# Kernel optimization log

Hardware: AMD Instinct MI355X
Metric: run time of the kernel (lower is better)

## Reference

```python
import jax, jax.numpy as jnp
import numpy as np

H = 2048       # hidden_size
I = 5504       # intermediate_size
E = 8          # num_experts
TOPK = 2       # num_experts_per_tok


def setup_inputs() -> dict:
    key = jax.random.key(0)
    ks = jax.random.split(key, 5)
    s = 0.02
    x = jax.random.normal(ks[0], (2, 2048, H), dtype=jnp.float32)
    router_w = jax.random.normal(ks[1], (E, H), dtype=jnp.float32) * s   # Linear weight [out,in]
    Wg = jax.random.normal(ks[2], (E, I, H), dtype=jnp.float32) * s      # gate_proj per expert
    Wu = jax.random.normal(ks[3], (E, I, H), dtype=jnp.float32) * s      # up_proj per expert
    Wd = jax.random.normal(ks[4], (E, H, I), dtype=jnp.float32) * s      # down_proj per expert
    return {"x": x, "router_w": router_w, "Wg": Wg, "Wu": Wu, "Wd": Wd}


def reference(x, router_w, Wg, Wu, Wd):
    B, S, Hh = x.shape
    xf = x.reshape(-1, Hh)                                  # [T, H]
    logits = xf @ router_w.T                                # [T, E]
    top_vals, top_idx = jax.lax.top_k(logits, TOPK)         # [T, K]
    top_w = jax.nn.softmax(top_vals, axis=-1)               # softmax over selected logits only
    # combine weight per (token, expert): zero if expert not selected
    combine = jnp.sum(jax.nn.one_hot(top_idx, E, dtype=xf.dtype) * top_w[..., None], axis=1)  # [T, E]

    out = jnp.zeros_like(xf)
    for e in range(E):  # fixed small expert loop (unrolled under jit)
        h = jax.nn.silu(xf @ Wg[e].T) * (xf @ Wu[e].T)      # [T, I]
        y = h @ Wd[e].T                                     # [T, H]
        out = out + combine[:, e:e + 1] * y
    return out.reshape(B, S, Hh)
```

## Files before the change

kernel.cpp:

```cpp
#include <hip/hip_runtime.h>
#include <cstdint>
#include <cstddef>

#define HDIM 2048
#define IDIM 5504
#define NEXP 8
#define NTOK 4096
#define NROWS (2 * NTOK)

#define NCT1 86
#define NRT1 10
#define NWG1 (NCT1 * NRT1 * NEXP)
#define NCT2 16
#define NRT2 10
#define NWG2 (NCT2 * NRT2 * NEXP)

typedef _Float16 half8 __attribute__((ext_vector_type(8)));
typedef _Float16 half4v __attribute__((ext_vector_type(4)));
typedef float floatx4 __attribute__((ext_vector_type(4)));

#define GLOAD16(g, l)                                                         \
  __builtin_amdgcn_global_load_lds(                                           \
      (const __attribute__((address_space(1))) void*)(g),                     \
      (__attribute__((address_space(3))) void*)(l), 16, 0, 0)

#define XH_OFF   0
#define HB_OFF   (XH_OFF + (size_t)NTOK * HDIM * 2)
#define BTOK_OFF (HB_OFF + (size_t)NROWS * IDIM * 2)
#define BW_OFF   (BTOK_OFF + 32768)
#define TOKP_OFF (BW_OFF + 32768)
#define TOKW_OFF (TOKP_OFF + 16384)
#define T2R_OFF  (TOKW_OFF + 32768)
#define META_OFF (T2R_OFF + 32768)
#define Y2_OFF   (META_OFF + 128)


__global__ void cvt_x_kernel(const float4* __restrict__ x, half4v* __restrict__ xh, int n4) {
  int i = blockIdx.x * blockDim.x + threadIdx.x;
  int st = gridDim.x * blockDim.x;
  for (; i < n4; i += st) {
    float4 v = x[i];
    half4v o = { (_Float16)v.x, (_Float16)v.y, (_Float16)v.z, (_Float16)v.w };
    xh[i] = o;
  }
}

__global__ void router_kernel(const float* __restrict__ x, const float* __restrict__ rw,
                              int* __restrict__ tokp, float2* __restrict__ tokw,
                              int* __restrict__ cnt) {
  int t = blockIdx.x * 4 + (threadIdx.x >> 6);
  int lane = threadIdx.x & 63;
  const float4* xr = (const float4*)(x + (size_t)t * HDIM);
  float acc[NEXP];
#pragma unroll
  for (int e = 0; e < NEXP; ++e) acc[e] = 0.f;
#pragma unroll
  for (int it = 0; it < HDIM / 256; ++it) {
    float4 xv = xr[lane + 64 * it];
#pragma unroll
    for (int e = 0; e < NEXP; ++e) {
      float4 wv = ((const float4*)(rw + (size_t)e * HDIM))[lane + 64 * it];
      acc[e] += xv.x * wv.x + xv.y * wv.y + xv.z * wv.z + xv.w * wv.w;
    }
  }
#pragma unroll
  for (int off = 32; off > 0; off >>= 1) {
#pragma unroll
    for (int e = 0; e < NEXP; ++e) acc[e] += __shfl_xor(acc[e], off);
  }
  if (lane == 0) {
    int e0 = 0; float v0 = acc[0];
#pragma unroll
    for (int e = 1; e < NEXP; ++e) {
      if (acc[e] > v0) { v0 = acc[e]; e0 = e; }
    }
    int e1 = -1; float v1 = -3.0e38f;
#pragma unroll
    for (int e = 0; e < NEXP; ++e) {
      if (e == e0) continue;
      if (acc[e] > v1) { v1 = acc[e]; e1 = e; }
    }
    float w0 = 1.f / (1.f + __expf(v1 - v0));
    tokp[t] = e0 | (e1 << 8);
    tokw[t] = make_float2(w0, 1.f - w0);
    atomicAdd(&cnt[e0], 1);
    atomicAdd(&cnt[e1], 1);
  }
}

__global__ void scan_kernel(const int* __restrict__ cnt, int* __restrict__ offp) {
  if (threadIdx.x == 0) {
    int s = 0;
    for (int e = 0; e < NEXP; ++e) { offp[e] = s; s += cnt[e]; }
    offp[NEXP] = s;
  }
}

__global__ void scatter_kernel(const int* __restrict__ tokp, const float2* __restrict__ tokw,
                               const int* __restrict__ offp, int* __restrict__ cursor,
                               int* __restrict__ btok, float* __restrict__ bw,
                               int* __restrict__ t2r) {
  int t = blockIdx.x * blockDim.x + threadIdx.x;
  if (t >= NTOK) return;
  int p = tokp[t];
  float2 w = tokw[t];
  int e0 = p & 0xff, e1 = (p >> 8) & 0xff;
  int r0 = offp[e0] + atomicAdd(&cursor[e0], 1);
  btok[r0] = t; bw[r0] = w.x; t2r[2 * t] = r0;
  int r1 = offp[e1] + atomicAdd(&cursor[e1], 1);
  btok[r1] = t; bw[r1] = w.y; t2r[2 * t + 1] = r1;
}

__global__ void combine_kernel(const _Float16* __restrict__ y2, const int* __restrict__ t2r,
                               const float2* __restrict__ tokw, float* __restrict__ out) {
  int idx = blockIdx.x * 256 + threadIdx.x;
  int t = idx >> 9, c = (idx & 511) * 4;
  int r0 = t2r[2 * t], r1 = t2r[2 * t + 1];
  float2 w = tokw[t];
  half4v v0 = *(const half4v*)(y2 + (size_t)r0 * HDIM + c);
  half4v v1 = *(const half4v*)(y2 + (size_t)r1 * HDIM + c);
  float4 o;
  o.x = w.x * (float)v0[0] + w.y * (float)v1[0];
  o.y = w.x * (float)v0[1] + w.y * (float)v1[1];
  o.z = w.x * (float)v0[2] + w.y * (float)v1[2];
  o.w = w.x * (float)v0[3] + w.y * (float)v1[3];
  *(float4*)(out + (size_t)t * HDIM + c) = o;
}

__global__ __launch_bounds__(256, 3) void stage1_kernel(
    const _Float16* __restrict__ xh, const float* __restrict__ Wg, const float* __restrict__ Wu,
    const int* __restrict__ offp, const int* __restrict__ btok, _Float16* __restrict__ hb) {
  int bid = blockIdx.x;
  int wg = (bid & 7) * (NWG1 / 8) + (bid >> 3);
  int rt = wg % NRT1;
  int ct = (wg / NRT1) % NCT1;
  int e  = wg / (NRT1 * NCT1);
  int base = offp[e];
  int ne = offp[e + 1] - base;
  if (rt * 128 >= ne) return;
  int valid = ne - rt * 128; if (valid > 128) valid = 128;
  int tid = threadIdx.x, lane = tid & 63, wave = tid >> 6;

  __shared__ __attribute__((aligned(16))) _Float16 As[2][128 * 32];
  __shared__ __attribute__((aligned(16))) _Float16 Bs[2][128 * 32];

  const char* abase = (const char*)xh;
  uint32_t aoffB[2];
  const float* bsrc[2];
  int bdstB[2];
  size_t eoff = (size_t)e * IDIM * HDIM;
#pragma unroll
  for (int i = 0; i < 2; ++i) {
    int L = wave * 128 + i * 64 + lane;
    int u = L >> 3, sc = (L & 7) ^ (u & 7);
    int r = 2 * u + (sc >> 2), q = sc & 3;
    int rr = (r < valid) ? r : (valid - 1);
    aoffB[i] = (uint32_t)(((uint32_t)btok[base + rt * 128 + rr] * HDIM + q * 8) * 2);
    const float* rp = (r < 64) ? (Wg + eoff + (size_t)(ct * 64 + r) * HDIM)
                               : (Wu + eoff + (size_t)(ct * 64 + (r - 64)) * HDIM);
    bsrc[i] = rp + q * 8;
    bdstB[i] = L * 16;
  }
  int adst0 = __builtin_amdgcn_readfirstlane(wave * 2048);

  int wm = wave >> 1, wn = wave & 1;
  int lrow = lane & 15, kg = lane >> 4;

  int aoff[4], boff[4];
#pragma unroll
  for (int mi = 0; mi < 4; ++mi) {
    int r = wm * 64 + mi * 16 + lrow;
    int u = r >> 1, cc = (r & 1) * 4 + kg;
    aoff[mi] = u * 64 + ((cc ^ (u & 7)) * 8);
  }
#pragma unroll
  for (int f = 0; f < 4; ++f) {
    int rb = (f < 2) ? (wn * 32 + f * 16 + lrow) : (64 + wn * 32 + (f - 2) * 16 + lrow);
    int u = rb >> 1, cc = (rb & 1) * 4 + kg;
    boff[f] = u * 64 + ((cc ^ (u & 7)) * 8);
  }

  floatx4 acc[4][4] = {};
  floatx4 bp[2][2];

  auto bload = [&](int t) {
#pragma unroll
    for (int i = 0; i < 2; ++i) {
      bp[i][0] = *(const floatx4*)(bsrc[i] + t * 32);
      bp[i][1] = *(const floatx4*)(bsrc[i] + t * 32 + 4);
    }
  };
  auto astage = [&](int t, int buf) {
    uint32_t kb = (uint32_t)t * 64u;
#pragma unroll
    for (int i = 0; i < 2; ++i)
      GLOAD16(abase + (aoffB[i] + kb), (char*)As[buf] + adst0 + i * 1024);
  };
  auto bwrite = [&](int buf) {
#pragma unroll
    for (int i = 0; i < 2; ++i) {
      half8 h = { (_Float16)bp[i][0].x, (_Float16)bp[i][0].y, (_Float16)bp[i][0].z, (_Float16)bp[i][0].w,
                  (_Float16)bp[i][1].x, (_Float16)bp[i][1].y, (_Float16)bp[i][1].z, (_Float16)bp[i][1].w };
      *(half8*)((char*)Bs[buf] + bdstB[i]) = h;
    }
  };
  auto compute = [&](int buf) {
    half8 af[4], bf[4];
#pragma unroll
    for (int mi = 0; mi < 4; ++mi) af[mi] = *(const half8*)&As[buf][aoff[mi]];
#pragma unroll
    for (int f = 0; f < 4; ++f) bf[f] = *(const half8*)&Bs[buf][boff[f]];
#pragma unroll
    for (int mi = 0; mi < 4; ++mi)
#pragma unroll
      for (int f = 0; f < 4; ++f)
        acc[mi][f] = __builtin_amdgcn_mfma_f32_16x16x32_f16(af[mi], bf[f], acc[mi][f], 0, 0, 0);
  };

  int cur = 0;
  bload(0);
  astage(0, 0);
  bwrite(0);
  __syncthreads();
#pragma unroll 2
  for (int t = 0; t < HDIM / 32 - 1; ++t) {
    bload(t + 1);
    astage(t + 1, cur ^ 1);
    compute(cur);
    bwrite(cur ^ 1);
    __syncthreads();
    cur ^= 1;
  }
  compute(cur);

  size_t hrow_base = (size_t)(base + rt * 128);
#pragma unroll
  for (int mi = 0; mi < 4; ++mi) {
#pragma unroll
    for (int j = 0; j < 4; ++j) {
      int r = wm * 64 + mi * 16 + kg * 4 + j;
      if (r < valid) {
#pragma unroll
        for (int f = 0; f < 2; ++f) {
          float g = acc[mi][f][j], u = acc[mi][f + 2][j];
          float hv = g / (1.f + __expf(-g)) * u;
          int c = ct * 64 + wn * 32 + f * 16 + lrow;
          hb[(hrow_base + r) * IDIM + c] = (_Float16)hv;
        }
      }
    }
  }
}

__global__ __launch_bounds__(256, 3) void stage2_kernel(
    const _Float16* __restrict__ hb, const float* __restrict__ Wd,
    const int* __restrict__ offp, _Float16* __restrict__ y2) {
  int bid = blockIdx.x;
  int wg = (bid & 7) * (NWG2 / 8) + (bid >> 3);
  int rt = wg % NRT2;
  int ct = (wg / NRT2) % NCT2;
  int e  = wg / (NRT2 * NCT2);
  int base = offp[e];
  int ne = offp[e + 1] - base;
  if (rt * 128 >= ne) return;
  int valid = ne - rt * 128; if (valid > 128) valid = 128;
  int tid = threadIdx.x, lane = tid & 63, wave = tid >> 6;

  __shared__ __attribute__((aligned(16))) _Float16 As[2][128 * 32];
  __shared__ __attribute__((aligned(16))) _Float16 Bs[2][128 * 32];

  const char* abase = (const char*)hb;
  uint32_t aoffB[2];
  const float* bsrc[2];
  int bdstB[2];
  const float* wdE = Wd + (size_t)e * HDIM * IDIM;
#pragma unroll
  for (int i = 0; i < 2; ++i) {
    int L = wave * 128 + i * 64 + lane;
    int u = L >> 3, sc = (L & 7) ^ (u & 7);
    int r = 2 * u + (sc >> 2), q = sc & 3;
    int rr = (r < valid) ? r : (valid - 1);
    aoffB[i] = (uint32_t)(((size_t)(base + rt * 128 + rr) * IDIM + (size_t)q * 8) * 2);
    bsrc[i] = wdE + (size_t)(ct * 128 + r) * IDIM + q * 8;
    bdstB[i] = L * 16;
  }
  int adst0 = __builtin_amdgcn_readfirstlane(wave * 2048);

  int wm = wave >> 1, wn = wave & 1;
  int lrow = lane & 15, kg = lane >> 4;

  int aoff[4], boff[4];
#pragma unroll
  for (int mi = 0; mi < 4; ++mi) {
    int r = wm * 64 + mi * 16 + lrow;
    int u = r >> 1, cc = (r & 1) * 4 + kg;
    aoff[mi] = u * 64 + ((cc ^ (u & 7)) * 8);
  }
#pragma unroll
  for (int f = 0; f < 4; ++f) {
    int rb = wn * 64 + f * 16 + lrow;
    int u = rb >> 1, cc = (rb & 1) * 4 + kg;
    boff[f] = u * 64 + ((cc ^ (u & 7)) * 8);
  }

  floatx4 acc[4][4] = {};
  floatx4 bp[2][2];

  auto bload = [&](int t) {
#pragma unroll
    for (int i = 0; i < 2; ++i) {
      bp[i][0] = *(const floatx4*)(bsrc[i] + t * 32);
      bp[i][1] = *(const floatx4*)(bsrc[i] + t * 32 + 4);
    }
  };
  auto astage = [&](int t, int buf) {
    uint32_t kb = (uint32_t)t * 64u;
#pragma unroll
    for (int i = 0; i < 2; ++i)
      GLOAD16(abase + (aoffB[i] + kb), (char*)As[buf] + adst0 + i * 1024);
  };
  auto bwrite = [&](int buf) {
#pragma unroll
    for (int i = 0; i < 2; ++i) {
      half8 h = { (_Float16)bp[i][0].x, (_Float16)bp[i][0].y, (_Float16)bp[i][0].z, (_Float16)bp[i][0].w,
                  (_Float16)bp[i][1].x, (_Float16)bp[i][1].y, (_Float16)bp[i][1].z, (_Float16)bp[i][1].w };
      *(half8*)((char*)Bs[buf] + bdstB[i]) = h;
    }
  };
  auto compute = [&](int buf) {
    half8 af[4], bf[4];
#pragma unroll
    for (int mi = 0; mi < 4; ++mi) af[mi] = *(const half8*)&As[buf][aoff[mi]];
#pragma unroll
    for (int f = 0; f < 4; ++f) bf[f] = *(const half8*)&Bs[buf][boff[f]];
#pragma unroll
    for (int mi = 0; mi < 4; ++mi)
#pragma unroll
      for (int f = 0; f < 4; ++f)
        acc[mi][f] = __builtin_amdgcn_mfma_f32_16x16x32_f16(af[mi], bf[f], acc[mi][f], 0, 0, 0);
  };

  int cur = 0;
  bload(0);
  astage(0, 0);
  bwrite(0);
  __syncthreads();
#pragma unroll 2
  for (int t = 0; t < IDIM / 32 - 1; ++t) {
    bload(t + 1);
    astage(t + 1, cur ^ 1);
    compute(cur);
    bwrite(cur ^ 1);
    __syncthreads();
    cur ^= 1;
  }
  compute(cur);

#pragma unroll
  for (int mi = 0; mi < 4; ++mi) {
#pragma unroll
    for (int j = 0; j < 4; ++j) {
      int r = wm * 64 + mi * 16 + kg * 4 + j;
      if (r < valid) {
        int grow = base + rt * 128 + r;
#pragma unroll
        for (int f = 0; f < 4; ++f) {
          int c = ct * 128 + wn * 64 + f * 16 + lrow;
          y2[(size_t)grow * HDIM + c] = (_Float16)acc[mi][f][j];
        }
      }
    }
  }
}

extern "C" void kernel_launch(void* const* d_in, const int* in_sizes, int n_in,
                              void* d_out, int out_size, void* d_ws, size_t ws_size,
                              hipStream_t stream) {
  const float* x  = (const float*)d_in[0];
  const float* rw = (const float*)d_in[1];
  const float* Wg = (const float*)d_in[2];
  const float* Wu = (const float*)d_in[3];
  const float* Wd = (const float*)d_in[4];
  float* out = (float*)d_out;

  char* ws = (char*)d_ws;
  _Float16* xh  = (_Float16*)(ws + XH_OFF);
  _Float16* hb  = (_Float16*)(ws + HB_OFF);
  int*      btok = (int*)(ws + BTOK_OFF);
  float*    bwv  = (float*)(ws + BW_OFF);
  int*      tokp = (int*)(ws + TOKP_OFF);
  float2*   tokw = (float2*)(ws + TOKW_OFF);
  int*      t2r  = (int*)(ws + T2R_OFF);
  int*      meta = (int*)(ws + META_OFF);
  _Float16* y2   = (_Float16*)(ws + Y2_OFF);
  int* cnt = meta;
  int* offp = meta + 8;
  int* cursor = meta + 20;

  hipMemsetAsync(meta, 0, 128, stream);

  cvt_x_kernel<<<2048, 256, 0, stream>>>((const float4*)x, (half4v*)xh, NTOK * HDIM / 4);
  router_kernel<<<NTOK / 4, 256, 0, stream>>>(x, rw, tokp, tokw, cnt);
  scan_kernel<<<1, 64, 0, stream>>>(cnt, offp);
  scatter_kernel<<<NTOK / 256, 256, 0, stream>>>(tokp, tokw, offp, cursor, btok, bwv, t2r);

  stage1_kernel<<<NWG1, 256, 0, stream>>>(xh, Wg, Wu, offp, btok, hb);
  stage2_kernel<<<NWG2, 256, 0, stream>>>(hb, Wd, offp, y2);
  combine_kernel<<<NTOK * HDIM / 4 / 256, 256, 0, stream>>>(y2, t2r, tokw, out);
}
```

Before: 1.227 ms.

## Prefetch B tiles two steps ahead with explicit waitcnt and barriers

Both GEMM kernels now keep two register buffers for the fp32 B tile, so global loads for tile t+2 are issued while tile t is being computed. The K loop is unrolled by two with fixed LDS buffer indices. The generic __syncthreads is replaced by hand-placed s_waitcnt vmcnt(4)/lgkmcnt(0) plus s_barrier, which lets the newest B loads stay in flight across the barrier. Loads past the end are clamped to the last tile, which adds a few redundant loads and uses more registers.

```diff
diff --git a/kernel.cpp b/kernel.cpp
--- a/kernel.cpp
+++ b/kernel.cpp
@@ -11,9 +11,11 @@
 #define NCT1 86
 #define NRT1 10
 #define NWG1 (NCT1 * NRT1 * NEXP)
+#define NK1  (HDIM / 32)
 #define NCT2 16
 #define NRT2 10
 #define NWG2 (NCT2 * NRT2 * NEXP)
+#define NK2  (IDIM / 32)
 
 typedef _Float16 half8 __attribute__((ext_vector_type(8)));
 typedef _Float16 half4v __attribute__((ext_vector_type(4)));
@@ -23,6 +25,10 @@
   __builtin_amdgcn_global_load_lds(                                           \
       (const __attribute__((address_space(1))) void*)(g),                     \
       (__attribute__((address_space(3))) void*)(l), 16, 0, 0)
+
+#define SBAR()   asm volatile("s_barrier" ::: "memory")
+#define VMCNT4() asm volatile("s_waitcnt vmcnt(4)" ::: "memory")
+#define LGKM0()  asm volatile("s_waitcnt lgkmcnt(0)" ::: "memory")
 
 #define XH_OFF   0
 #define HB_OFF   (XH_OFF + (size_t)NTOK * HDIM * 2)
@@ -181,22 +187,24 @@
   }
 
   floatx4 acc[4][4] = {};
-  floatx4 bp[2][2];
-
-  auto bload = [&](int t) {
+  floatx4 bpE[2][2], bpO[2][2];
+
+  auto bload = [&](int t, floatx4 (&bp)[2][2]) {
+    int tc = (t < NK1) ? t : NK1 - 1;
 #pragma unroll
     for (int i = 0; i < 2; ++i) {
-      bp[i][0] = *(const floatx4*)(bsrc[i] + t * 32);
-      bp[i][1] = *(const floatx4*)(bsrc[i] + t * 32 + 4);
+      bp[i][0] = *(const floatx4*)(bsrc[i] + tc * 32);
+      bp[i][1] = *(const floatx4*)(bsrc[i] + tc * 32 + 4);
     }
   };
   auto astage = [&](int t, int buf) {
-    uint32_t kb = (uint32_t)t * 64u;
+    int tc = (t < NK1) ? t : NK1 - 1;
+    uint32_t kb = (uint32_t)tc * 64u;
 #pragma unroll
     for (int i = 0; i < 2; ++i)
       GLOAD16(abase + (aoffB[i] + kb), (char*)As[buf] + adst0 + i * 1024);
   };
-  auto bwrite = [&](int buf) {
+  auto bwrite = [&](floatx4 (&bp)[2][2], int buf) {
 #pragma unroll
     for (int i = 0; i < 2; ++i) {
       half8 h = { (_Float16)bp[i][0].x, (_Float16)bp[i][0].y, (_Float16)bp[i][0].z, (_Float16)bp[i][0].w,
@@ -204,12 +212,12 @@
       *(half8*)((char*)Bs[buf] + bdstB[i]) = h;
     }
   };
-  auto compute = [&](int buf) {
+  auto compute = [&](int abuf, int bbuf) {
     half8 af[4], bf[4];
 #pragma unroll
-    for (int mi = 0; mi < 4; ++mi) af[mi] = *(const half8*)&As[buf][aoff[mi]];
-#pragma unroll
-    for (int f = 0; f < 4; ++f) bf[f] = *(const half8*)&Bs[buf][boff[f]];
+    for (int mi = 0; mi < 4; ++mi) af[mi] = *(const half8*)&As[abuf][aoff[mi]];
+#pragma unroll
+    for (int f = 0; f < 4; ++f) bf[f] = *(const half8*)&Bs[bbuf][boff[f]];
 #pragma unroll
     for (int mi = 0; mi < 4; ++mi)
 #pragma unroll
@@ -217,21 +225,25 @@
         acc[mi][f] = __builtin_amdgcn_mfma_f32_16x16x32_f16(af[mi], bf[f], acc[mi][f], 0, 0, 0);
   };
 
-  int cur = 0;
-  bload(0);
   astage(0, 0);
-  bwrite(0);
-  __syncthreads();
-#pragma unroll 2
-  for (int t = 0; t < HDIM / 32 - 1; ++t) {
-    bload(t + 1);
-    astage(t + 1, cur ^ 1);
-    compute(cur);
-    bwrite(cur ^ 1);
-    __syncthreads();
-    cur ^= 1;
-  }
-  compute(cur);
+  bload(0, bpE);
+  bload(1, bpO);
+  bwrite(bpE, 0);
+  LGKM0(); SBAR();
+
+  for (int I = 0; I < NK1 / 2; ++I) {
+    int t0 = 2 * I, t1 = 2 * I + 1;
+    astage(t0 + 1, 1);
+    compute(0, 0);
+    bwrite(bpO, 1);
+    bload(t0 + 2, bpE);
+    VMCNT4(); LGKM0(); SBAR();
+    astage(t1 + 1, 0);
+    compute(1, 1);
+    bwrite(bpE, 0);
+    bload(t1 + 2, bpO);
+    VMCNT4(); LGKM0(); SBAR();
+  }
 
   size_t hrow_base = (size_t)(base + rt * 128);
 #pragma unroll
@@ -304,22 +316,24 @@
   }
 
   floatx4 acc[4][4] = {};
-  floatx4 bp[2][2];
-
-  auto bload = [&](int t) {
+  floatx4 bpE[2][2], bpO[2][2];
+
+  auto bload = [&](int t, floatx4 (&bp)[2][2]) {
+    int tc = (t < NK2) ? t : NK2 - 1;
 #pragma unroll
     for (int i = 0; i < 2; ++i) {
-      bp[i][0] = *(const floatx4*)(bsrc[i] + t * 32);
-      bp[i][1] = *(const floatx4*)(bsrc[i] + t * 32 + 4);
+      bp[i][0] = *(const floatx4*)(bsrc[i] + tc * 32);
+      bp[i][1] = *(const floatx4*)(bsrc[i] + tc * 32 + 4);
     }
   };
   auto astage = [&](int t, int buf) {
-    uint32_t kb = (uint32_t)t * 64u;
+    int tc = (t < NK2) ? t : NK2 - 1;
+    uint32_t kb = (uint32_t)tc * 64u;
 #pragma unroll
     for (int i = 0; i < 2; ++i)
       GLOAD16(abase + (aoffB[i] + kb), (char*)As[buf] + adst0 + i * 1024);
   };
-  auto bwrite = [&](int buf) {
+  auto bwrite = [&](floatx4 (&bp)[2][2], int buf) {
 #pragma unroll
     for (int i = 0; i < 2; ++i) {
       half8 h = { (_Float16)bp[i][0].x, (_Float16)bp[i][0].y, (_Float16)bp[i][0].z, (_Float16)bp[i][0].w,
@@ -327,12 +341,12 @@
       *(half8*)((char*)Bs[buf] + bdstB[i]) = h;
     }
   };
-  auto compute = [&](int buf) {
+  auto compute = [&](int abuf, int bbuf) {
     half8 af[4], bf[4];
 #pragma unroll
-    for (int mi = 0; mi < 4; ++mi) af[mi] = *(const half8*)&As[buf][aoff[mi]];
-#pragma unroll
-    for (int f = 0; f < 4; ++f) bf[f] = *(const half8*)&Bs[buf][boff[f]];
+    for (int mi = 0; mi < 4; ++mi) af[mi] = *(const half8*)&As[abuf][aoff[mi]];
+#pragma unroll
+    for (int f = 0; f < 4; ++f) bf[f] = *(const half8*)&Bs[bbuf][boff[f]];
 #pragma unroll
     for (int mi = 0; mi < 4; ++mi)
 #pragma unroll
@@ -340,21 +354,25 @@
         acc[mi][f] = __builtin_amdgcn_mfma_f32_16x16x32_f16(af[mi], bf[f], acc[mi][f], 0, 0, 0);
   };
 
-  int cur = 0;
-  bload(0);
   astage(0, 0);
-  bwrite(0);
-  __syncthreads();
-#pragma unroll 2
-  for (int t = 0; t < IDIM / 32 - 1; ++t) {
-    bload(t + 1);
-    astage(t + 1, cur ^ 1);
-    compute(cur);
-    bwrite(cur ^ 1);
-    __syncthreads();
-    cur ^= 1;
-  }
-  compute(cur);
+  bload(0, bpE);
+  bload(1, bpO);
+  bwrite(bpE, 0);
+  LGKM0(); SBAR();
+
+  for (int I = 0; I < NK2 / 2; ++I) {
+    int t0 = 2 * I, t1 = 2 * I + 1;
+    astage(t0 + 1, 1);
+    compute(0, 0);
+    bwrite(bpO, 1);
+    bload(t0 + 2, bpE);
+    VMCNT4(); LGKM0(); SBAR();
+    astage(t1 + 1, 0);
+    compute(1, 1);
+    bwrite(bpE, 0);
+    bload(t1 + 2, bpO);
+    VMCNT4(); LGKM0(); SBAR();
+  }
 
 #pragma unroll
   for (int mi = 0; mi < 4; ++mi) {
```

Measured after the change: 1.240 ms. Within noise of the previous version (+1.0%).

## Pre-convert down-proj weights to fp16 and fuse x conversion into router

Applied to the files above, without the earlier changes.

Adds a pass that converts all of Wd to fp16 in workspace each call, so stage2 can stream B tiles directly into LDS with async global-to-LDS loads instead of loading fp32 into registers and converting. The separate x-to-fp16 kernel is removed and folded into the router, which already reads x. This trades an extra full pass over Wd (about 360MB read, 180MB written) for a simpler, fully asynchronous stage2 pipeline with half the B bytes per tile. Stage2 is re-read per row tile, so the fp16 copy may cut its repeated reads.

```diff
diff --git a/kernel.cpp b/kernel.cpp
--- a/kernel.cpp
+++ b/kernel.cpp
@@ -11,9 +11,11 @@
 #define NCT1 86
 #define NRT1 10
 #define NWG1 (NCT1 * NRT1 * NEXP)
+#define NK1  (HDIM / 32)
 #define NCT2 16
 #define NRT2 10
 #define NWG2 (NCT2 * NRT2 * NEXP)
+#define NK2  (IDIM / 32)
 
 typedef _Float16 half8 __attribute__((ext_vector_type(8)));
 typedef _Float16 half4v __attribute__((ext_vector_type(4)));
@@ -33,30 +35,35 @@
 #define T2R_OFF  (TOKW_OFF + 32768)
 #define META_OFF (T2R_OFF + 32768)
 #define Y2_OFF   (META_OFF + 128)
-
-
-__global__ void cvt_x_kernel(const float4* __restrict__ x, half4v* __restrict__ xh, int n4) {
+#define WD16_OFF (Y2_OFF + (size_t)NROWS * HDIM * 2)
+
+
+__global__ void cvt_w_kernel(const float4* __restrict__ w, half8* __restrict__ o, int n8) {
   int i = blockIdx.x * blockDim.x + threadIdx.x;
   int st = gridDim.x * blockDim.x;
-  for (; i < n4; i += st) {
-    float4 v = x[i];
-    half4v o = { (_Float16)v.x, (_Float16)v.y, (_Float16)v.z, (_Float16)v.w };
-    xh[i] = o;
+  for (; i < n8; i += st) {
+    float4 a = w[2 * i], b = w[2 * i + 1];
+    o[i] = half8{ (_Float16)a.x, (_Float16)a.y, (_Float16)a.z, (_Float16)a.w,
+                  (_Float16)b.x, (_Float16)b.y, (_Float16)b.z, (_Float16)b.w };
   }
 }
 
 __global__ void router_kernel(const float* __restrict__ x, const float* __restrict__ rw,
+                              _Float16* __restrict__ xh,
                               int* __restrict__ tokp, float2* __restrict__ tokw,
                               int* __restrict__ cnt) {
   int t = blockIdx.x * 4 + (threadIdx.x >> 6);
   int lane = threadIdx.x & 63;
   const float4* xr = (const float4*)(x + (size_t)t * HDIM);
+  _Float16* xhr = xh + (size_t)t * HDIM;
   float acc[NEXP];
 #pragma unroll
   for (int e = 0; e < NEXP; ++e) acc[e] = 0.f;
 #pragma unroll
   for (int it = 0; it < HDIM / 256; ++it) {
     float4 xv = xr[lane + 64 * it];
+    half4v hv = { (_Float16)xv.x, (_Float16)xv.y, (_Float16)xv.z, (_Float16)xv.w };
+    *(half4v*)(xhr + (lane + 64 * it) * 4) = hv;
 #pragma unroll
     for (int e = 0; e < NEXP; ++e) {
       float4 wv = ((const float4*)(rw + (size_t)e * HDIM))[lane + 64 * it];
@@ -223,7 +230,7 @@
   bwrite(0);
   __syncthreads();
 #pragma unroll 2
-  for (int t = 0; t < HDIM / 32 - 1; ++t) {
+  for (int t = 0; t < NK1 - 1; ++t) {
     bload(t + 1);
     astage(t + 1, cur ^ 1);
     compute(cur);
@@ -253,7 +260,7 @@
 }
 
 __global__ __launch_bounds__(256, 3) void stage2_kernel(
-    const _Float16* __restrict__ hb, const float* __restrict__ Wd,
+    const _Float16* __restrict__ hb, const _Float16* __restrict__ Wd16,
     const int* __restrict__ offp, _Float16* __restrict__ y2) {
   int bid = blockIdx.x;
   int wg = (bid & 7) * (NWG2 / 8) + (bid >> 3);
@@ -270,10 +277,9 @@
   __shared__ __attribute__((aligned(16))) _Float16 Bs[2][128 * 32];
 
   const char* abase = (const char*)hb;
-  uint32_t aoffB[2];
-  const float* bsrc[2];
-  int bdstB[2];
-  const float* wdE = Wd + (size_t)e * HDIM * IDIM;
+  const char* bbase = (const char*)(Wd16 + (size_t)e * HDIM * IDIM);
+
+  uint32_t aoffB[2], boffB[2];
 #pragma unroll
   for (int i = 0; i < 2; ++i) {
     int L = wave * 128 + i * 64 + lane;
@@ -281,8 +287,7 @@
     int r = 2 * u + (sc >> 2), q = sc & 3;
     int rr = (r < valid) ? r : (valid - 1);
     aoffB[i] = (uint32_t)(((size_t)(base + rt * 128 + rr) * IDIM + (size_t)q * 8) * 2);
-    bsrc[i] = wdE + (size_t)(ct * 128 + r) * IDIM + q * 8;
-    bdstB[i] = L * 16;
+    boffB[i] = (uint32_t)(((size_t)(ct * 128 + r) * IDIM + (size_t)q * 8) * 2);
   }
   int adst0 = __builtin_amdgcn_readfirstlane(wave * 2048);
 
@@ -304,27 +309,13 @@
   }
 
   floatx4 acc[4][4] = {};
-  floatx4 bp[2][2];
-
-  auto bload = [&](int t) {
+
+  auto stage = [&](int t, int buf) {
+    uint32_t kb = (uint32_t)t * 64u;
 #pragma unroll
     for (int i = 0; i < 2; ++i) {
-      bp[i][0] = *(const floatx4*)(bsrc[i] + t * 32);
-      bp[i][1] = *(const floatx4*)(bsrc[i] + t * 32 + 4);
-    }
-  };
-  auto astage = [&](int t, int buf) {
-    uint32_t kb = (uint32_t)t * 64u;
-#pragma unroll
-    for (int i = 0; i < 2; ++i)
       GLOAD16(abase + (aoffB[i] + kb), (char*)As[buf] + adst0 + i * 1024);
-  };
-  auto bwrite = [&](int buf) {
-#pragma unroll
-    for (int i = 0; i < 2; ++i) {
-      half8 h = { (_Float16)bp[i][0].x, (_Float16)bp[i][0].y, (_Float16)bp[i][0].z, (_Float16)bp[i][0].w,
-                  (_Float16)bp[i][1].x, (_Float16)bp[i][1].y, (_Float16)bp[i][1].z, (_Float16)bp[i][1].w };
-      *(half8*)((char*)Bs[buf] + bdstB[i]) = h;
+      GLOAD16(bbase + (boffB[i] + kb), (char*)Bs[buf] + adst0 + i * 1024);
     }
   };
   auto compute = [&](int buf) {
@@ -341,16 +332,12 @@
   };
 
   int cur = 0;
-  bload(0);
-  astage(0, 0);
-  bwrite(0);
+  stage(0, 0);
   __syncthreads();
 #pragma unroll 2
-  for (int t = 0; t < IDIM / 32 - 1; ++t) {
-    bload(t + 1);
-    astage(t + 1, cur ^ 1);
+  for (int t = 0; t < NK2 - 1; ++t) {
+    stage(t + 1, cur ^ 1);
     compute(cur);
-    bwrite(cur ^ 1);
     __syncthreads();
     cur ^= 1;
   }
@@ -393,18 +380,20 @@
   int*      t2r  = (int*)(ws + T2R_OFF);
   int*      meta = (int*)(ws + META_OFF);
   _Float16* y2   = (_Float16*)(ws + Y2_OFF);
+  _Float16* wd16 = (_Float16*)(ws + WD16_OFF);
   int* cnt = meta;
   int* offp = meta + 8;
   int* cursor = meta + 20;
 
   hipMemsetAsync(meta, 0, 128, stream);
 
-  cvt_x_kernel<<<2048, 256, 0, stream>>>((const float4*)x, (half4v*)xh, NTOK * HDIM / 4);
-  router_kernel<<<NTOK / 4, 256, 0, stream>>>(x, rw, tokp, tokw, cnt);
+  router_kernel<<<NTOK / 4, 256, 0, stream>>>(x, rw, xh, tokp, tokw, cnt);
   scan_kernel<<<1, 64, 0, stream>>>(cnt, offp);
   scatter_kernel<<<NTOK / 256, 256, 0, stream>>>(tokp, tokw, offp, cursor, btok, bwv, t2r);
+  cvt_w_kernel<<<2048, 256, 0, stream>>>((const float4*)Wd, (half8*)wd16,
+                                         NEXP * HDIM * IDIM / 8);
 
   stage1_kernel<<<NWG1, 256, 0, stream>>>(xh, Wg, Wu, offp, btok, hb);
-  stage2_kernel<<<NWG2, 256, 0, stream>>>(hb, Wd, offp, y2);
+  stage2_kernel<<<NWG2, 256, 0, stream>>>(hb, wd16, offp, y2);
   combine_kernel<<<NTOK * HDIM / 4 / 256, 256, 0, stream>>>(y2, t2r, tokw, out);
 }
```

After: 1.156 ms, median of 2. -5.8%, faster.
